# Kernel tuning notes

Measured on AMD Instinct MI355X. Metric: run time of the kernel, lower is better.

Reference implementation:

```python
import math
import jax, jax.numpy as jnp
import numpy as np

VMIN, VMAX = 0.0, 1.0
NUM_BINS = 64
SIGMA = 0.5 * (VMAX - VMIN) / NUM_BINS  # matches torch: sigma * (vmax-vmin)/num_bins
EPS = 1e-10


def setup_inputs() -> dict:
    key = jax.random.key(0)
    k1, k2 = jax.random.split(key)
    shape = (2, 1, 96, 96, 96)
    tar = jax.random.uniform(k1, shape, dtype=jnp.float32)
    src = jax.random.uniform(k2, shape, dtype=jnp.float32)
    return {"tar": tar, "src": src}


def _normalise_minmax(x, min_out, max_out):
    # x: (N, P) -- per-sample min-max normalisation to [min_out, max_out]
    xmin = jnp.min(x, axis=1, keepdims=True)
    xmax = jnp.max(x, axis=1, keepdims=True)
    return (x - xmin) / (xmax - xmin + EPS) * (max_out - min_out) + min_out


def _windowed(x, bins):
    # x: (N, P), bins: (B,) -> (N, B, P) Gaussian kernel weights
    d = x[:, None, :] - bins[None, :, None]
    return jnp.exp(-(d * d) / (2.0 * SIGMA * SIGMA)) / math.sqrt(2.0 * math.pi) * SIGMA


def reference(tar, src):
    N = tar.shape[0]
    # use channel 0 only, flatten spatial dims
    t = _normalise_minmax(tar[:, 0].reshape(N, -1), VMIN, VMAX)
    s = _normalise_minmax(src[:, 0].reshape(N, -1), VMIN, VMAX)

    bins = jnp.linspace(VMIN, VMAX, NUM_BINS, dtype=tar.dtype)
    w_tar = _windowed(t, bins)  # (N, B, P)
    w_src = _windowed(s, bins)  # (N, B, P)

    hist_joint = jnp.einsum('nbp,ncp->nbc', w_tar, w_src)  # (N, B, B)
    hist_norm = jnp.sum(hist_joint, axis=(1, 2), keepdims=True)
    p_joint = hist_joint / hist_norm

    p_tar = jnp.sum(p_joint, axis=2)  # (N, B)
    p_src = jnp.sum(p_joint, axis=1)  # (N, B)

    ent_tar = -jnp.sum(p_tar * jnp.log(p_tar + EPS), axis=1)
    ent_src = -jnp.sum(p_src * jnp.log(p_src + EPS), axis=1)
    ent_joint = -jnp.sum(p_joint * jnp.log(p_joint + EPS), axis=(1, 2))

    # normalised=True branch
    return -jnp.mean((ent_tar + ent_src) / ent_joint)
```

## Files before the change

kernel.cpp:

```cpp
#include <hip/hip_runtime.h>
#include <math.h>

#define NBINS 64
#define HIST_ELEMS (NBINS*NBINS)
#define PTS_PER_BLOCK 3456
#define GXN 256
#define CHUNKS 27
#define LSTRIDE 68
#define SQK 1.7256062f

typedef float f4 __attribute__((ext_vector_type(4)));
typedef float f32x4 __attribute__((ext_vector_type(4)));
typedef _Float16 half8 __attribute__((ext_vector_type(8)));
typedef int int4v __attribute__((ext_vector_type(4)));

static __device__ __forceinline__ unsigned f2key(float f) {
    unsigned u = __float_as_uint(f);
    return (u & 0x80000000u) ? ~u : (u | 0x80000000u);
}
static __device__ __forceinline__ float key2f(unsigned u) {
    return (u & 0x80000000u) ? __uint_as_float(u & 0x7fffffffu) : __uint_as_float(~u);
}

static __device__ __forceinline__ half8 pack8(const float* w) {
    int4v v;
    v[0] = __builtin_bit_cast(int, __builtin_amdgcn_cvt_pkrtz(w[0], w[1]));
    v[1] = __builtin_bit_cast(int, __builtin_amdgcn_cvt_pkrtz(w[2], w[3]));
    v[2] = __builtin_bit_cast(int, __builtin_amdgcn_cvt_pkrtz(w[4], w[5]));
    v[3] = __builtin_bit_cast(int, __builtin_amdgcn_cvt_pkrtz(w[6], w[7]));
    return __builtin_bit_cast(half8, v);
}

__global__ __launch_bounds__(256) void minmax_kernel(const float* __restrict__ tar,
                                                     const float* __restrict__ src,
                                                     unsigned* __restrict__ mm, int P) {
    const int n = blockIdx.y;
    const int t = blockIdx.z;
    const f4* x = (const f4*)((t == 0 ? tar : src) + (size_t)n * P);
    const int n4 = P / 4;
    float lmin = INFINITY, lmax = -INFINITY;
    for (int i = blockIdx.x * blockDim.x + threadIdx.x; i < n4; i += gridDim.x * blockDim.x) {
        f4 v = x[i];
        lmin = fminf(lmin, fminf(fminf(v[0], v[1]), fminf(v[2], v[3])));
        lmax = fmaxf(lmax, fmaxf(fmaxf(v[0], v[1]), fmaxf(v[2], v[3])));
    }
    for (int off = 32; off > 0; off >>= 1) {
        lmin = fminf(lmin, __shfl_down(lmin, off, 64));
        lmax = fmaxf(lmax, __shfl_down(lmax, off, 64));
    }
    __shared__ float smin[4], smax[4];
    const int lane = threadIdx.x & 63, wave = threadIdx.x >> 6;
    if (lane == 0) { smin[wave] = lmin; smax[wave] = lmax; }
    __syncthreads();
    if (threadIdx.x == 0) {
        float m = fminf(fminf(smin[0], smin[1]), fminf(smin[2], smin[3]));
        float M = fmaxf(fmaxf(smax[0], smax[1]), fmaxf(smax[2], smax[3]));
        atomicMin(&mm[n * 2 + t], f2key(m));
        atomicMin(&mm[4 + n * 2 + t], ~f2key(M));
    }
}

template <int STAGED>
__global__ __launch_bounds__(256) void mfma_hist_kernel(const float* __restrict__ tar,
                                                        const float* __restrict__ src,
                                                        const unsigned* __restrict__ mm,
                                                        float* __restrict__ bh,
                                                        float* __restrict__ hist,
                                                        int P) {
    const int n = blockIdx.y;
    const int bx = blockIdx.x;
    const int tid = threadIdx.x;
    const int lane = tid & 63, wave = tid >> 6;
    const int mlane = lane & 15, quad = lane >> 4;

    __shared__ float su_t[PTS_PER_BLOCK], su_s[PTS_PER_BLOCK];
    __shared__ float lh[NBINS * LSTRIDE];

    const float tmin = key2f(mm[n * 2 + 0]);
    const float tmax = key2f(~mm[4 + n * 2 + 0]);
    const float smin = key2f(mm[n * 2 + 1]);
    const float smax = key2f(~mm[4 + n * 2 + 1]);
    const float tk = 63.0f / (tmax - tmin + 1e-10f) * SQK;
    const float sk = 63.0f / (smax - smin + 1e-10f) * SQK;
    const float toff = tmin * tk, soff = smin * sk;

    {
        const f4* tg = (const f4*)(tar + (size_t)n * P + (size_t)bx * PTS_PER_BLOCK);
        const f4* sg = (const f4*)(src + (size_t)n * P + (size_t)bx * PTS_PER_BLOCK);
        f4* st4 = (f4*)su_t;
        f4* ss4 = (f4*)su_s;
        #pragma unroll
        for (int k = 0; k < 3; ++k) {
            const int i = tid + k * 256;
            f4 tv = tg[i], sv = sg[i];
            f4 utv, usv;
            #pragma unroll
            for (int c = 0; c < 4; ++c) {
                utv[c] = fmaf(tv[c], tk, -toff);
                usv[c] = fmaf(sv[c], sk, -soff);
            }
            st4[i] = utv;
            ss4[i] = usv;
        }
        if (tid < 96) {
            const int i = 768 + tid;
            f4 tv = tg[i], sv = sg[i];
            f4 utv, usv;
            #pragma unroll
            for (int c = 0; c < 4; ++c) {
                utv[c] = fmaf(tv[c], tk, -toff);
                usv[c] = fmaf(sv[c], sk, -soff);
            }
            st4[i] = utv;
            ss4[i] = usv;
        }
    }
    __syncthreads();

    float mhat[4];
    #pragma unroll
    for (int mt = 0; mt < 4; ++mt) mhat[mt] = (float)(mlane + 16 * mt) * SQK;

    f32x4 acc[4][4];
    #pragma unroll
    for (int a = 0; a < 4; ++a)
        #pragma unroll
        for (int b = 0; b < 4; ++b) acc[a][b] = (f32x4){0.f, 0.f, 0.f, 0.f};

    const int kwbase = wave * (32 * CHUNKS) + quad * 8;
    #pragma unroll 3
    for (int c = 0; c < CHUNKS; ++c) {
        const int kbase = kwbase + c * 32;
        const f4* pt4 = (const f4*)&su_t[kbase];
        const f4* ps4 = (const f4*)&su_s[kbase];
        f4 ta = pt4[0], tb = pt4[1];
        f4 sa = ps4[0], sb = ps4[1];
        float ut[8] = {ta[0], ta[1], ta[2], ta[3], tb[0], tb[1], tb[2], tb[3]};
        float us[8] = {sa[0], sa[1], sa[2], sa[3], sb[0], sb[1], sb[2], sb[3]};

        half8 af[4], bf[4];
        #pragma unroll
        for (int mt = 0; mt < 4; ++mt) {
            float w[8];
            #pragma unroll
            for (int j = 0; j < 8; ++j) {
                float d = ut[j] - mhat[mt];
                w[j] = __builtin_amdgcn_exp2f(-(d * d));
            }
            af[mt] = pack8(w);
        }
        #pragma unroll
        for (int nt = 0; nt < 4; ++nt) {
            float w[8];
            #pragma unroll
            for (int j = 0; j < 8; ++j) {
                float d = us[j] - mhat[nt];
                w[j] = __builtin_amdgcn_exp2f(-(d * d));
            }
            bf[nt] = pack8(w);
        }
        #pragma unroll
        for (int mt = 0; mt < 4; ++mt)
            #pragma unroll
            for (int nt = 0; nt < 4; ++nt)
                acc[mt][nt] = __builtin_amdgcn_mfma_f32_16x16x32_f16(
                    af[mt], bf[nt], acc[mt][nt], 0, 0, 0);
    }

    #pragma unroll
    for (int w = 0; w < 4; ++w) {
        if (wave == w) {
            #pragma unroll
            for (int nt = 0; nt < 4; ++nt)
                #pragma unroll
                for (int mt = 0; mt < 4; ++mt) {
                    f4* p = (f4*)&lh[(16 * nt + mlane) * LSTRIDE + 16 * mt + 4 * quad];
                    if (w == 0) {
                        *p = acc[mt][nt];
                    } else {
                        f4 v = *p;
                        v += acc[mt][nt];
                        *p = v;
                    }
                }
        }
        __syncthreads();
    }

    if (STAGED) {
        f4* dst = (f4*)(bh + ((size_t)n * GXN + bx) * HIST_ELEMS);
        #pragma unroll
        for (int k = 0; k < 4; ++k) {
            const int i4 = tid + k * 256;
            const int c = i4 >> 4, r4 = (i4 & 15) * 4;
            dst[i4] = *(const f4*)&lh[c * LSTRIDE + r4];
        }
    } else {
        float* gh = hist + (size_t)n * HIST_ELEMS;
        for (int i = tid; i < HIST_ELEMS; i += 256) {
            const int c = i >> 6, r = i & 63;
            unsafeAtomicAdd(&gh[i], lh[c * LSTRIDE + r]);
        }
    }
}

__global__ __launch_bounds__(256) void reduce_kernel(const float* __restrict__ bh,
                                                     float* __restrict__ hist) {
    const int g = blockIdx.x * 256 + threadIdx.x;
    const int n = g >> 12, e = g & 4095;
    const float* p = bh + ((size_t)n * GXN) * HIST_ELEMS + e;
    float sum = 0.0f;
    #pragma unroll 8
    for (int b = 0; b < GXN; ++b) sum += p[(size_t)b * HIST_ELEMS];
    hist[g] = sum;
}

static __device__ __forceinline__ float block_reduce_sum(float v, float* buf) {
    for (int off = 32; off > 0; off >>= 1) v += __shfl_down(v, off, 64);
    const int lane = threadIdx.x & 63, wave = threadIdx.x >> 6;
    __syncthreads();
    if (lane == 0) buf[wave] = v;
    __syncthreads();
    return buf[0] + buf[1] + buf[2] + buf[3];
}

__global__ __launch_bounds__(256) void finalize_kernel(const float* __restrict__ ghist,
                                                       float* __restrict__ out) {
    __shared__ float buf[4];
    __shared__ float colp[4][NBINS];
    __shared__ float rowsum[NBINS], colsum[NBINS];
    const int tid = threadIdx.x;
    float acc = 0.0f;
    for (int n = 0; n < 2; ++n) {
        const float* h = ghist + n * HIST_ELEMS;
        {
            int r = tid >> 2, q = tid & 3;
            const float* hp = h + r * NBINS + q * 16;
            float sv = 0.0f;
            #pragma unroll
            for (int k = 0; k < 16; ++k) sv += hp[k];
            sv += __shfl_down(sv, 1, 64);
            sv += __shfl_down(sv, 2, 64);
            if (q == 0) rowsum[r] = sv;
        }
        {
            int c = tid & 63, g = tid >> 6;
            const float* hp = h + (g * 16) * NBINS + c;
            float sv = 0.0f;
            #pragma unroll
            for (int k = 0; k < 16; ++k) sv += hp[k * NBINS];
            colp[g][c] = sv;
        }
        __syncthreads();
        if (tid < NBINS)
            colsum[tid] = colp[0][tid] + colp[1][tid] + colp[2][tid] + colp[3][tid];
        __syncthreads();

        float tv = (tid < NBINS) ? rowsum[tid] : 0.0f;
        float total = block_reduce_sum(tv, buf);
        float inv = 1.0f / total;

        float ej = 0.0f;
        for (int i = tid; i < HIST_ELEMS; i += 256) {
            float p = h[i] * inv;
            ej += p * __logf(p + 1e-10f);
        }
        float entj = -block_reduce_sum(ej, buf);

        float em = 0.0f;
        if (tid < NBINS) {
            float p = rowsum[tid] * inv;
            em = p * __logf(p + 1e-10f);
        } else if (tid < 2 * NBINS) {
            float p = colsum[tid - NBINS] * inv;
            em = p * __logf(p + 1e-10f);
        }
        float ents = -block_reduce_sum(em, buf);

        acc += ents / entj;
        __syncthreads();
    }
    if (tid == 0) out[0] = -0.5f * acc;
}

extern "C" void kernel_launch(void* const* d_in, const int* in_sizes, int n_in,
                              void* d_out, int out_size, void* d_ws, size_t ws_size,
                              hipStream_t stream) {
    const float* tar = (const float*)d_in[0];
    const float* src = (const float*)d_in[1];
    const int N = 2;
    const int P = in_sizes[0] / N;

    unsigned* mm = (unsigned*)d_ws;
    float* hist = (float*)((char*)d_ws + 256);
    float* bh = (float*)((char*)d_ws + 256 + 2 * HIST_ELEMS * sizeof(float));
    float* out = (float*)d_out;

    const size_t need = 256 + (size_t)2 * HIST_ELEMS * 4 + (size_t)2 * GXN * HIST_ELEMS * 4;

    hipMemsetAsync(d_ws, 0xFF, 32, stream);
    minmax_kernel<<<dim3(128, N, 2), 256, 0, stream>>>(tar, src, mm, P);
    if (ws_size >= need) {
        mfma_hist_kernel<1><<<dim3(GXN, N), 256, 0, stream>>>(tar, src, mm, bh, hist, P);
        reduce_kernel<<<32, 256, 0, stream>>>(bh, hist);
    } else {
        hipMemsetAsync((char*)d_ws + 256, 0x00, 2 * HIST_ELEMS * sizeof(float), stream);
        mfma_hist_kernel<0><<<dim3(GXN, N), 256, 0, stream>>>(tar, src, mm, bh, hist, P);
    }
    finalize_kernel<<<1, 256, 0, stream>>>(hist, out);
}
```

Measured before the change: 138.0 us.

## Fuse histogram reduction and finalize into hist kernel via last-block pattern

Folds the memsets, staged per-block histogram buffer, reduce kernel and finalize kernel into two launches. The minmax kernel now writes per-block partial min/max and zeroes the global histogram and a counter. The histogram kernel reduces those partials itself, folds the normalisation into the per-bin FMA, and accumulates into the global histogram with atomics. The last block to finish, found through an atomic counter, computes the entropies. This removes launch overhead and the large staged buffer round trip, at the cost of atomic contention on 8K floats from 512 blocks.

```diff
diff --git a/kernel.cpp b/kernel.cpp
--- a/kernel.cpp
+++ b/kernel.cpp
@@ -5,22 +5,16 @@
 #define HIST_ELEMS (NBINS*NBINS)
 #define PTS_PER_BLOCK 3456
 #define GXN 256
+#define TOTAL_HBLOCKS (GXN*2)
 #define CHUNKS 27
 #define LSTRIDE 68
 #define SQK 1.7256062f
+#define SMEM_FLOATS (2*PTS_PER_BLOCK + NBINS*LSTRIDE)
 
 typedef float f4 __attribute__((ext_vector_type(4)));
 typedef float f32x4 __attribute__((ext_vector_type(4)));
 typedef _Float16 half8 __attribute__((ext_vector_type(8)));
 typedef int int4v __attribute__((ext_vector_type(4)));
-
-static __device__ __forceinline__ unsigned f2key(float f) {
-    unsigned u = __float_as_uint(f);
-    return (u & 0x80000000u) ? ~u : (u | 0x80000000u);
-}
-static __device__ __forceinline__ float key2f(unsigned u) {
-    return (u & 0x80000000u) ? __uint_as_float(u & 0x7fffffffu) : __uint_as_float(~u);
-}
 
 static __device__ __forceinline__ half8 pack8(const float* w) {
     int4v v;
@@ -33,13 +27,14 @@
 
 __global__ __launch_bounds__(256) void minmax_kernel(const float* __restrict__ tar,
                                                      const float* __restrict__ src,
-                                                     unsigned* __restrict__ mm, int P) {
-    const int n = blockIdx.y;
-    const int t = blockIdx.z;
+                                                     float* __restrict__ pm,
+                                                     unsigned* __restrict__ ctr,
+                                                     float* __restrict__ hist, int P) {
+    const int b = blockIdx.x, n = blockIdx.y, t = blockIdx.z;
     const f4* x = (const f4*)((t == 0 ? tar : src) + (size_t)n * P);
-    const int n4 = P / 4;
+    const int per = (P / 4) / 64;
     float lmin = INFINITY, lmax = -INFINITY;
-    for (int i = blockIdx.x * blockDim.x + threadIdx.x; i < n4; i += gridDim.x * blockDim.x) {
+    for (int i = b * per + threadIdx.x; i < (b + 1) * per; i += 256) {
         f4 v = x[i];
         lmin = fminf(lmin, fminf(fminf(v[0], v[1]), fminf(v[2], v[3])));
         lmax = fmaxf(lmax, fmaxf(fmaxf(v[0], v[1]), fmaxf(v[2], v[3])));
@@ -53,36 +48,48 @@
     if (lane == 0) { smin[wave] = lmin; smax[wave] = lmax; }
     __syncthreads();
     if (threadIdx.x == 0) {
-        float m = fminf(fminf(smin[0], smin[1]), fminf(smin[2], smin[3]));
-        float M = fmaxf(fmaxf(smax[0], smax[1]), fmaxf(smax[2], smax[3]));
-        atomicMin(&mm[n * 2 + t], f2key(m));
-        atomicMin(&mm[4 + n * 2 + t], ~f2key(M));
-    }
-}
-
-template <int STAGED>
-__global__ __launch_bounds__(256) void mfma_hist_kernel(const float* __restrict__ tar,
-                                                        const float* __restrict__ src,
-                                                        const unsigned* __restrict__ mm,
-                                                        float* __restrict__ bh,
-                                                        float* __restrict__ hist,
-                                                        int P) {
+        pm[(n * 2 + t) * 64 + b] =
+            fminf(fminf(smin[0], smin[1]), fminf(smin[2], smin[3]));
+        pm[256 + (n * 2 + t) * 64 + b] =
+            fmaxf(fmaxf(smax[0], smax[1]), fmaxf(smax[2], smax[3]));
+    }
+    const int flat = b + 64 * n + 128 * t;
+    if (threadIdx.x < 32) hist[flat * 32 + threadIdx.x] = 0.0f;
+    if (flat == 0 && threadIdx.x == 0) *ctr = 0u;
+}
+
+__global__ __launch_bounds__(256) void mfma_hist_fused(const float* __restrict__ tar,
+                                                       const float* __restrict__ src,
+                                                       const float* __restrict__ pm,
+                                                       unsigned* __restrict__ ctr,
+                                                       float* __restrict__ hist,
+                                                       float* __restrict__ out, int P) {
     const int n = blockIdx.y;
     const int bx = blockIdx.x;
     const int tid = threadIdx.x;
     const int lane = tid & 63, wave = tid >> 6;
     const int mlane = lane & 15, quad = lane >> 4;
 
-    __shared__ float su_t[PTS_PER_BLOCK], su_s[PTS_PER_BLOCK];
-    __shared__ float lh[NBINS * LSTRIDE];
-
-    const float tmin = key2f(mm[n * 2 + 0]);
-    const float tmax = key2f(~mm[4 + n * 2 + 0]);
-    const float smin = key2f(mm[n * 2 + 1]);
-    const float smax = key2f(~mm[4 + n * 2 + 1]);
-    const float tk = 63.0f / (tmax - tmin + 1e-10f) * SQK;
-    const float sk = 63.0f / (smax - smin + 1e-10f) * SQK;
-    const float toff = tmin * tk, soff = smin * sk;
+    __shared__ float smem[SMEM_FLOATS];
+    __shared__ float mmred[4];
+    __shared__ int lastflag;
+    float* su_t = smem;
+    float* su_s = smem + PTS_PER_BLOCK;
+    float* lh = smem + 2 * PTS_PER_BLOCK;
+
+    if (wave == 0) {
+        float a = pm[(n * 2 + 0) * 64 + lane];
+        float b = pm[256 + (n * 2 + 0) * 64 + lane];
+        float c = pm[(n * 2 + 1) * 64 + lane];
+        float d = pm[256 + (n * 2 + 1) * 64 + lane];
+        for (int off = 32; off > 0; off >>= 1) {
+            a = fminf(a, __shfl_down(a, off, 64));
+            b = fmaxf(b, __shfl_down(b, off, 64));
+            c = fminf(c, __shfl_down(c, off, 64));
+            d = fmaxf(d, __shfl_down(d, off, 64));
+        }
+        if (lane == 0) { mmred[0] = a; mmred[1] = b; mmred[2] = c; mmred[3] = d; }
+    }
 
     {
         const f4* tg = (const f4*)(tar + (size_t)n * P + (size_t)bx * PTS_PER_BLOCK);
@@ -92,34 +99,28 @@
         #pragma unroll
         for (int k = 0; k < 3; ++k) {
             const int i = tid + k * 256;
-            f4 tv = tg[i], sv = sg[i];
-            f4 utv, usv;
-            #pragma unroll
-            for (int c = 0; c < 4; ++c) {
-                utv[c] = fmaf(tv[c], tk, -toff);
-                usv[c] = fmaf(sv[c], sk, -soff);
-            }
-            st4[i] = utv;
-            ss4[i] = usv;
+            st4[i] = tg[i];
+            ss4[i] = sg[i];
         }
         if (tid < 96) {
             const int i = 768 + tid;
-            f4 tv = tg[i], sv = sg[i];
-            f4 utv, usv;
-            #pragma unroll
-            for (int c = 0; c < 4; ++c) {
-                utv[c] = fmaf(tv[c], tk, -toff);
-                usv[c] = fmaf(sv[c], sk, -soff);
-            }
-            st4[i] = utv;
-            ss4[i] = usv;
-        }
-    }
-    __syncthreads();
-
-    float mhat[4];
+            st4[i] = tg[i];
+            ss4[i] = sg[i];
+        }
+    }
+    __syncthreads();
+
+    const float tmin = mmred[0], tmax = mmred[1];
+    const float smin = mmred[2], smax = mmred[3];
+    const float tk = 63.0f / (tmax - tmin + 1e-10f) * SQK;
+    const float sk = 63.0f / (smax - smin + 1e-10f) * SQK;
+    float mt2[4], ms2[4];
     #pragma unroll
-    for (int mt = 0; mt < 4; ++mt) mhat[mt] = (float)(mlane + 16 * mt) * SQK;
+    for (int mt = 0; mt < 4; ++mt) {
+        const float b = SQK * (float)(mlane + 16 * mt);
+        mt2[mt] = tmin * tk + b;
+        ms2[mt] = smin * sk + b;
+    }
 
     f32x4 acc[4][4];
     #pragma unroll
@@ -135,8 +136,8 @@
         const f4* ps4 = (const f4*)&su_s[kbase];
         f4 ta = pt4[0], tb = pt4[1];
         f4 sa = ps4[0], sb = ps4[1];
-        float ut[8] = {ta[0], ta[1], ta[2], ta[3], tb[0], tb[1], tb[2], tb[3]};
-        float us[8] = {sa[0], sa[1], sa[2], sa[3], sb[0], sb[1], sb[2], sb[3]};
+        float xt[8] = {ta[0], ta[1], ta[2], ta[3], tb[0], tb[1], tb[2], tb[3]};
+        float xs[8] = {sa[0], sa[1], sa[2], sa[3], sb[0], sb[1], sb[2], sb[3]};
 
         half8 af[4], bf[4];
         #pragma unroll
@@ -144,7 +145,7 @@
             float w[8];
             #pragma unroll
             for (int j = 0; j < 8; ++j) {
-                float d = ut[j] - mhat[mt];
+                float d = fmaf(xt[j], tk, -mt2[mt]);
                 w[j] = __builtin_amdgcn_exp2f(-(d * d));
             }
             af[mt] = pack8(w);
@@ -154,7 +155,7 @@
             float w[8];
             #pragma unroll
             for (int j = 0; j < 8; ++j) {
-                float d = us[j] - mhat[nt];
+                float d = fmaf(xs[j], sk, -ms2[nt]);
                 w[j] = __builtin_amdgcn_exp2f(-(d * d));
             }
             bf[nt] = pack8(w);
@@ -187,52 +188,32 @@
         __syncthreads();
     }
 
-    if (STAGED) {
-        f4* dst = (f4*)(bh + ((size_t)n * GXN + bx) * HIST_ELEMS);
-        #pragma unroll
-        for (int k = 0; k < 4; ++k) {
-            const int i4 = tid + k * 256;
-            const int c = i4 >> 4, r4 = (i4 & 15) * 4;
-            dst[i4] = *(const f4*)&lh[c * LSTRIDE + r4];
-        }
-    } else {
-        float* gh = hist + (size_t)n * HIST_ELEMS;
-        for (int i = tid; i < HIST_ELEMS; i += 256) {
-            const int c = i >> 6, r = i & 63;
-            unsafeAtomicAdd(&gh[i], lh[c * LSTRIDE + r]);
-        }
-    }
-}
-
-__global__ __launch_bounds__(256) void reduce_kernel(const float* __restrict__ bh,
-                                                     float* __restrict__ hist) {
-    const int g = blockIdx.x * 256 + threadIdx.x;
-    const int n = g >> 12, e = g & 4095;
-    const float* p = bh + ((size_t)n * GXN) * HIST_ELEMS + e;
-    float sum = 0.0f;
-    #pragma unroll 8
-    for (int b = 0; b < GXN; ++b) sum += p[(size_t)b * HIST_ELEMS];
-    hist[g] = sum;
-}
-
-static __device__ __forceinline__ float block_reduce_sum(float v, float* buf) {
-    for (int off = 32; off > 0; off >>= 1) v += __shfl_down(v, off, 64);
-    const int lane = threadIdx.x & 63, wave = threadIdx.x >> 6;
-    __syncthreads();
-    if (lane == 0) buf[wave] = v;
-    __syncthreads();
-    return buf[0] + buf[1] + buf[2] + buf[3];
-}
-
-__global__ __launch_bounds__(256) void finalize_kernel(const float* __restrict__ ghist,
-                                                       float* __restrict__ out) {
-    __shared__ float buf[4];
-    __shared__ float colp[4][NBINS];
-    __shared__ float rowsum[NBINS], colsum[NBINS];
-    const int tid = threadIdx.x;
-    float acc = 0.0f;
-    for (int n = 0; n < 2; ++n) {
-        const float* h = ghist + n * HIST_ELEMS;
+    float* gh = hist + (size_t)n * HIST_ELEMS;
+    for (int i = tid; i < HIST_ELEMS; i += 256) {
+        const int c = i >> 6, r = i & 63;
+        unsafeAtomicAdd(&gh[i], lh[c * LSTRIDE + r]);
+    }
+
+    __threadfence();
+    if (tid == 0) {
+        unsigned old = atomicAdd(ctr, 1u);
+        lastflag = (old == TOTAL_HBLOCKS - 1) ? 1 : 0;
+    }
+    __syncthreads();
+    if (!lastflag) return;
+    __threadfence();
+
+    for (int i = tid; i < 2 * HIST_ELEMS; i += 256)
+        smem[i] = __hip_atomic_load(&hist[i], __ATOMIC_RELAXED, __HIP_MEMORY_SCOPE_AGENT);
+    __syncthreads();
+
+    float* buf    = smem + 2 * HIST_ELEMS;
+    float* rowsum = smem + 2 * HIST_ELEMS + 4;
+    float* colsum = smem + 2 * HIST_ELEMS + 68;
+    float* colp   = smem + 2 * HIST_ELEMS + 132;
+    float accl = 0.0f;
+    for (int nn = 0; nn < 2; ++nn) {
+        const float* h = smem + nn * HIST_ELEMS;
         {
             int r = tid >> 2, q = tid & 3;
             const float* hp = h + r * NBINS + q * 16;
@@ -249,23 +230,32 @@
             float sv = 0.0f;
             #pragma unroll
             for (int k = 0; k < 16; ++k) sv += hp[k * NBINS];
-            colp[g][c] = sv;
+            colp[g * NBINS + c] = sv;
         }
         __syncthreads();
         if (tid < NBINS)
-            colsum[tid] = colp[0][tid] + colp[1][tid] + colp[2][tid] + colp[3][tid];
+            colsum[tid] = colp[0 * NBINS + tid] + colp[1 * NBINS + tid] +
+                          colp[2 * NBINS + tid] + colp[3 * NBINS + tid];
         __syncthreads();
 
         float tv = (tid < NBINS) ? rowsum[tid] : 0.0f;
-        float total = block_reduce_sum(tv, buf);
-        float inv = 1.0f / total;
+        for (int off = 32; off > 0; off >>= 1) tv += __shfl_down(tv, off, 64);
+        __syncthreads();
+        if (lane == 0) buf[wave] = tv;
+        __syncthreads();
+        const float total = buf[0] + buf[1] + buf[2] + buf[3];
+        const float inv = 1.0f / total;
 
         float ej = 0.0f;
         for (int i = tid; i < HIST_ELEMS; i += 256) {
             float p = h[i] * inv;
             ej += p * __logf(p + 1e-10f);
         }
-        float entj = -block_reduce_sum(ej, buf);
+        for (int off = 32; off > 0; off >>= 1) ej += __shfl_down(ej, off, 64);
+        __syncthreads();
+        if (lane == 0) buf[wave] = ej;
+        __syncthreads();
+        const float entj = -(buf[0] + buf[1] + buf[2] + buf[3]);
 
         float em = 0.0f;
         if (tid < NBINS) {
@@ -275,12 +265,16 @@
             float p = colsum[tid - NBINS] * inv;
             em = p * __logf(p + 1e-10f);
         }
-        float ents = -block_reduce_sum(em, buf);
-
-        acc += ents / entj;
-        __syncthreads();
-    }
-    if (tid == 0) out[0] = -0.5f * acc;
+        for (int off = 32; off > 0; off >>= 1) em += __shfl_down(em, off, 64);
+        __syncthreads();
+        if (lane == 0) buf[wave] = em;
+        __syncthreads();
+        const float ents = -(buf[0] + buf[1] + buf[2] + buf[3]);
+
+        accl += ents / entj;
+        __syncthreads();
+    }
+    if (tid == 0) out[0] = -0.5f * accl;
 }
 
 extern "C" void kernel_launch(void* const* d_in, const int* in_sizes, int n_in,
@@ -291,21 +285,11 @@
     const int N = 2;
     const int P = in_sizes[0] / N;
 
-    unsigned* mm = (unsigned*)d_ws;
-    float* hist = (float*)((char*)d_ws + 256);
-    float* bh = (float*)((char*)d_ws + 256 + 2 * HIST_ELEMS * sizeof(float));
+    float* pm = (float*)d_ws;
+    unsigned* ctr = (unsigned*)((char*)d_ws + 2048);
+    float* hist = (float*)((char*)d_ws + 4096);
     float* out = (float*)d_out;
 
-    const size_t need = 256 + (size_t)2 * HIST_ELEMS * 4 + (size_t)2 * GXN * HIST_ELEMS * 4;
-
-    hipMemsetAsync(d_ws, 0xFF, 32, stream);
-    minmax_kernel<<<dim3(128, N, 2), 256, 0, stream>>>(tar, src, mm, P);
-    if (ws_size >= need) {
-        mfma_hist_kernel<1><<<dim3(GXN, N), 256, 0, stream>>>(tar, src, mm, bh, hist, P);
-        reduce_kernel<<<32, 256, 0, stream>>>(bh, hist);
-    } else {
-        hipMemsetAsync((char*)d_ws + 256, 0x00, 2 * HIST_ELEMS * sizeof(float), stream);
-        mfma_hist_kernel<0><<<dim3(GXN, N), 256, 0, stream>>>(tar, src, mm, bh, hist, P);
-    }
-    finalize_kernel<<<1, 256, 0, stream>>>(hist, out);
-}
+    minmax_kernel<<<dim3(64, N, 2), 256, 0, stream>>>(tar, src, pm, ctr, hist, P);
+    mfma_hist_fused<<<dim3(GXN, N), 256, 0, stream>>>(tar, src, pm, ctr, hist, out, P);
+}
```

Result: no change. 137.5 us (-0.4%).
